# Performance work log

Measured on AMD Instinct MI355X. Metric: run time of the kernel, lower is better.

## Reference

```python
import jax, jax.numpy as jnp
import numpy as np

B, K, F, C = 256, 16, 128, 2
EPS = 1e-5


def setup_inputs() -> dict:
    key = jax.random.key(0)
    ks = jax.random.split(key, 16)
    n = lambda k, shape, s=1.0: (jax.random.normal(k, shape, dtype=jnp.float32) * s)
    return {
        "x0": n(ks[0], (B, F)),
        "x1": n(ks[1], (B, K, F)),
        "x2": n(ks[2], (B, K * K, F)),
        "x3": n(ks[3], (B, K ** 3, F)),
        "W0": n(ks[4], (2 * F, F), 0.05), "b0": n(ks[5], (F,), 0.05),
        "W1": n(ks[6], (2 * F, F), 0.05), "b1": n(ks[7], (F,), 0.05),
        "W2": n(ks[8], (2 * F, F), 0.05), "b2": n(ks[9], (F,), 0.05),
        "lin1_W": n(ks[10], (F, 8), 0.05), "lin1_b": n(ks[11], (8,), 0.05),
        "bn_gamma": jnp.ones((8,), jnp.float32), "bn_beta": jnp.zeros((8,), jnp.float32),
        "lin2_W": n(ks[12], (8, C), 0.05), "lin2_b": n(ks[13], (C,), 0.05),
    }


def _agg_mean(x):
    # block-wise mean over groups of K along dim 1: [B, N, F] -> [B, N//K, F]
    b, n_, f = x.shape
    return x.reshape(b, n_ // K, K, f).mean(axis=2)


def reference(x0, x1, x2, x3, W0, b0, W1, b1, W2, b2,
              lin1_W, lin1_b, bn_gamma, bn_beta, lin2_W, lin2_b):
    # layer i=3: mean-agg x3 blocks, concat with x2, Linear(2F->F)+ReLU
    h2 = jax.nn.relu(jnp.concatenate([_agg_mean(x3), x2], axis=2) @ W2 + b2)
    # layer i=2
    h1 = jax.nn.relu(jnp.concatenate([_agg_mean(h2), x1], axis=2) @ W1 + b1)
    # layer i=1: agg gives [B,1,F]; squeeze and concat along feature dim
    h0 = jax.nn.relu(jnp.concatenate([_agg_mean(h1)[:, 0, :], x0], axis=1) @ W0 + b0)
    # classifier head: Linear -> BatchNorm1d (training batch stats) -> Linear -> Sigmoid
    z = h0 @ lin1_W + lin1_b                       # [B, 8]
    mu = z.mean(axis=0)
    var = jnp.mean(jnp.square(z - mu), axis=0)     # biased var, as torch BN
    zn = (z - mu) * jax.lax.rsqrt(var + EPS) * bn_gamma + bn_beta
    return jax.nn.sigmoid(zn @ lin2_W + lin2_b)    # [B, C]
```

## Files before the change

kernel.cpp:

```cpp
#include <hip/hip_runtime.h>
#include <math.h>

#define NTHR 256

typedef __bf16 bf16x8 __attribute__((ext_vector_type(8)));
typedef float  f32x4  __attribute__((ext_vector_type(4)));

__device__ __forceinline__ unsigned short f2bf(float x) {
    unsigned int u = __float_as_uint(x);
    return (unsigned short)((u + 0x7fffu + ((u >> 16) & 1u)) >> 16);
}
__device__ __forceinline__ ushort4 pack4(float a, float b, float c, float d) {
    return make_ushort4(f2bf(a), f2bf(b), f2bf(c), f2bf(d));
}

template<int TM>
__global__ __launch_bounds__(NTHR, 3)
void layer_kernel(const float* __restrict__ deep,
                  const float* __restrict__ shallow,
                  const float* __restrict__ W,
                  const float* __restrict__ bias,
                  float* __restrict__ out)
{
    constexpr int MT = TM / 16;
    __shared__ unsigned short A[TM][264];
    const int t  = threadIdx.x;
    const int m0 = blockIdx.x * TM;

    {
        const int r8 = t >> 5;
        const int l  = t & 31;
        const int fo = l * 4;
        for (int rr = r8; rr < TM; rr += 8) {
            const int m = m0 + rr;
            const float4* dp = (const float4*)(deep + (size_t)m * 2048 + fo);
            float4 s = dp[0];
            #pragma unroll
            for (int k = 1; k < 16; ++k) {
                float4 v = dp[k * 32];
                s.x += v.x; s.y += v.y; s.z += v.z; s.w += v.w;
            }
            const float inv = 1.0f / 16.0f;
            float4 sh = *(const float4*)(shallow + (size_t)m * 128 + fo);
            *(ushort4*)&A[rr][fo]       = pack4(s.x * inv, s.y * inv, s.z * inv, s.w * inv);
            *(ushort4*)&A[rr][128 + fo] = pack4(sh.x, sh.y, sh.z, sh.w);
        }
    }

    const int l    = t & 63;
    const int w    = t >> 6;
    const int lo16 = l & 15;
    const int q    = l >> 4;
    const int c0   = w * 32;

    bf16x8 Bf[16];
    #pragma unroll
    for (int kt = 0; kt < 8; ++kt) {
        #pragma unroll
        for (int nt = 0; nt < 2; ++nt) {
            const float* p = W + (size_t)(kt * 32 + q * 8) * 128 + c0 + nt * 16 + lo16;
            union { unsigned short u[8]; bf16x8 v; } tmp;
            #pragma unroll
            for (int j = 0; j < 8; ++j) tmp.u[j] = f2bf(p[(size_t)j * 128]);
            Bf[kt * 2 + nt] = tmp.v;
        }
    }
    __syncthreads();

    f32x4 acc[MT][2];
    #pragma unroll
    for (int mt = 0; mt < MT; ++mt) {
        acc[mt][0] = (f32x4){0.f, 0.f, 0.f, 0.f};
        acc[mt][1] = (f32x4){0.f, 0.f, 0.f, 0.f};
    }

    #pragma unroll
    for (int kt = 0; kt < 8; ++kt) {
        #pragma unroll
        for (int mt = 0; mt < MT; ++mt) {
            bf16x8 Af = *(const bf16x8*)&A[mt * 16 + lo16][kt * 32 + q * 8];
            acc[mt][0] = __builtin_amdgcn_mfma_f32_16x16x32_bf16(Af, Bf[kt * 2 + 0], acc[mt][0], 0, 0, 0);
            acc[mt][1] = __builtin_amdgcn_mfma_f32_16x16x32_bf16(Af, Bf[kt * 2 + 1], acc[mt][1], 0, 0, 0);
        }
    }

    const float bn0 = bias[c0 + lo16];
    const float bn1 = bias[c0 + 16 + lo16];
    #pragma unroll
    for (int mt = 0; mt < MT; ++mt) {
        #pragma unroll
        for (int r = 0; r < 4; ++r) {
            const int row = m0 + mt * 16 + q * 4 + r;
            float* op = out + (size_t)row * 128;
            op[c0 + lo16]      = fmaxf(acc[mt][0][r] + bn0, 0.0f);
            op[c0 + 16 + lo16] = fmaxf(acc[mt][1][r] + bn1, 0.0f);
        }
    }
}

__global__ __launch_bounds__(NTHR)
void head_kernel(const float* __restrict__ h0,
                 const float* __restrict__ l1W,
                 const float* __restrict__ l1b,
                 const float* __restrict__ gamma,
                 const float* __restrict__ beta,
                 const float* __restrict__ l2W,
                 const float* __restrict__ l2b,
                 float* __restrict__ out)
{
    __shared__ float z[256][8];
    __shared__ float w1s[128 * 8];
    __shared__ float ps[32][8];
    __shared__ float pq[32][8];
    __shared__ float scale_s[8], shift_s[8];

    const int t  = threadIdx.x;
    const int j  = t & 7;
    const int rg = t >> 3;

    #pragma unroll
    for (int i = 0; i < 4; ++i) w1s[t * 4 + i] = l1W[t * 4 + i];
    __syncthreads();

    const float bj = l1b[j];
    for (int it = 0; it < 8; ++it) {
        const int b = it * 32 + rg;
        const float4* hr = (const float4*)(h0 + (size_t)b * 128);
        float s = bj;
        #pragma unroll
        for (int f4 = 0; f4 < 32; ++f4) {
            float4 h = hr[f4];
            s += h.x * w1s[(f4 * 4 + 0) * 8 + j];
            s += h.y * w1s[(f4 * 4 + 1) * 8 + j];
            s += h.z * w1s[(f4 * 4 + 2) * 8 + j];
            s += h.w * w1s[(f4 * 4 + 3) * 8 + j];
        }
        z[b][j] = s;
    }
    __syncthreads();

    {
        float s = 0.0f, qq = 0.0f;
        #pragma unroll
        for (int r = 0; r < 8; ++r) {
            float v = z[rg * 8 + r][j];
            s += v; qq += v * v;
        }
        ps[rg][j] = s; pq[rg][j] = qq;
    }
    __syncthreads();

    if (t < 8) {
        float s = 0.0f, qq = 0.0f;
        #pragma unroll
        for (int p = 0; p < 32; ++p) { s += ps[p][t]; qq += pq[p][t]; }
        const float mu  = s * (1.0f / 256.0f);
        const float var = qq * (1.0f / 256.0f) - mu * mu;
        const float sc  = gamma[t] * rsqrtf(var + 1e-5f);
        scale_s[t] = sc;
        shift_s[t] = beta[t] - mu * sc;
    }
    __syncthreads();

    {
        float o0 = l2b[0], o1 = l2b[1];
        #pragma unroll
        for (int jj = 0; jj < 8; ++jj) {
            const float zn = z[t][jj] * scale_s[jj] + shift_s[jj];
            o0 += zn * l2W[jj * 2 + 0];
            o1 += zn * l2W[jj * 2 + 1];
        }
        out[t * 2 + 0] = 1.0f / (1.0f + expf(-o0));
        out[t * 2 + 1] = 1.0f / (1.0f + expf(-o1));
    }
}

extern "C" void kernel_launch(void* const* d_in, const int* in_sizes, int n_in,
                              void* d_out, int out_size, void* d_ws, size_t ws_size,
                              hipStream_t stream)
{
    const float* x0    = (const float*)d_in[0];
    const float* x1    = (const float*)d_in[1];
    const float* x2    = (const float*)d_in[2];
    const float* x3    = (const float*)d_in[3];
    const float* W0    = (const float*)d_in[4];
    const float* b0    = (const float*)d_in[5];
    const float* W1    = (const float*)d_in[6];
    const float* b1    = (const float*)d_in[7];
    const float* W2    = (const float*)d_in[8];
    const float* b2    = (const float*)d_in[9];
    const float* l1W   = (const float*)d_in[10];
    const float* l1b   = (const float*)d_in[11];
    const float* gamma = (const float*)d_in[12];
    const float* beta  = (const float*)d_in[13];
    const float* l2W   = (const float*)d_in[14];
    const float* l2b   = (const float*)d_in[15];
    float* out = (float*)d_out;

    float* h2 = (float*)d_ws;
    float* h1 = h2 + (size_t)65536 * 128;
    float* h0 = h1 + (size_t)4096 * 128;

    hipLaunchKernelGGL((layer_kernel<64>), dim3(65536 / 64), dim3(NTHR), 0, stream,
                       x3, x2, W2, b2, h2);
    hipLaunchKernelGGL((layer_kernel<16>), dim3(4096 / 16), dim3(NTHR), 0, stream,
                       h2, x1, W1, b1, h1);
    hipLaunchKernelGGL((layer_kernel<16>), dim3(256 / 16), dim3(NTHR), 0, stream,
                       h1, x0, W0, b0, h0);
    hipLaunchKernelGGL(head_kernel, dim3(1), dim3(NTHR), 0, stream,
                       h0, l1W, l1b, gamma, beta, l2W, l2b, out);
}
```

Baseline: 761.8 us.

## Fuse downstream mean-aggregation into layer epilogues and use nontemporal loads

Each layer now reduces its ReLU outputs over groups of 16 rows inside the MFMA epilogue, using cross-lane shuffles, and writes only the group means. This removes the full h2/h1 intermediate writes and the 16x re-read in the next layer. The x3 stream is read with nontemporal loads, and occupancy hint rises to 4 blocks. Later layers use 64-row tiles, so launch grids are much smaller (64 and 4 blocks), which limits parallelism for those stages.

After: 732.7 us. -3.8%, faster.

```diff
diff --git a/kernel.cpp b/kernel.cpp
--- a/kernel.cpp
+++ b/kernel.cpp
@@ -5,22 +5,26 @@
 
 typedef __bf16 bf16x8 __attribute__((ext_vector_type(8)));
 typedef float  f32x4  __attribute__((ext_vector_type(4)));
+typedef float  f32x4v __attribute__((ext_vector_type(4)));
 
 __device__ __forceinline__ unsigned short f2bf(float x) {
     unsigned int u = __float_as_uint(x);
     return (unsigned short)((u + 0x7fffu + ((u >> 16) & 1u)) >> 16);
 }
-__device__ __forceinline__ ushort4 pack4(float a, float b, float c, float d) {
-    return make_ushort4(f2bf(a), f2bf(b), f2bf(c), f2bf(d));
-}
-
-template<int TM>
-__global__ __launch_bounds__(NTHR, 3)
+__device__ __forceinline__ ushort4 pack4v(f32x4v v) {
+    return make_ushort4(f2bf(v[0]), f2bf(v[1]), f2bf(v[2]), f2bf(v[3]));
+}
+__device__ __forceinline__ f32x4v ntload4(const float* p) {
+    return __builtin_nontemporal_load((const f32x4v*)p);
+}
+
+template<int TM, bool AGG_IN, bool AGG_OUT>
+__global__ __launch_bounds__(NTHR, 4)
 void layer_kernel(const float* __restrict__ deep,
-                  const float* __restrict__ shallow,
+                  const float* __restrict__ shal,
                   const float* __restrict__ W,
                   const float* __restrict__ bias,
-                  float* __restrict__ out)
+                  float* __restrict__ outp)
 {
     constexpr int MT = TM / 16;
     __shared__ unsigned short A[TM][264];
@@ -33,17 +37,20 @@
         const int fo = l * 4;
         for (int rr = r8; rr < TM; rr += 8) {
             const int m = m0 + rr;
-            const float4* dp = (const float4*)(deep + (size_t)m * 2048 + fo);
-            float4 s = dp[0];
-            #pragma unroll
-            for (int k = 1; k < 16; ++k) {
-                float4 v = dp[k * 32];
-                s.x += v.x; s.y += v.y; s.z += v.z; s.w += v.w;
+            f32x4v s, sh;
+            if (AGG_IN) {
+                const float* dp = deep + (size_t)m * 2048 + fo;
+                s = ntload4(dp);
+                #pragma unroll
+                for (int k = 1; k < 16; ++k) s += ntload4(dp + k * 128);
+                s *= (1.0f / 16.0f);
+                sh = ntload4(shal + (size_t)m * 128 + fo);
+            } else {
+                s  = *(const f32x4v*)(deep + (size_t)m * 128 + fo);
+                sh = *(const f32x4v*)(shal + (size_t)m * 128 + fo);
             }
-            const float inv = 1.0f / 16.0f;
-            float4 sh = *(const float4*)(shallow + (size_t)m * 128 + fo);
-            *(ushort4*)&A[rr][fo]       = pack4(s.x * inv, s.y * inv, s.z * inv, s.w * inv);
-            *(ushort4*)&A[rr][128 + fo] = pack4(sh.x, sh.y, sh.z, sh.w);
+            *(ushort4*)&A[rr][fo]       = pack4v(s);
+            *(ushort4*)&A[rr][128 + fo] = pack4v(sh);
         }
     }
 
@@ -73,7 +80,6 @@
         acc[mt][0] = (f32x4){0.f, 0.f, 0.f, 0.f};
         acc[mt][1] = (f32x4){0.f, 0.f, 0.f, 0.f};
     }
-
     #pragma unroll
     for (int kt = 0; kt < 8; ++kt) {
         #pragma unroll
@@ -86,14 +92,31 @@
 
     const float bn0 = bias[c0 + lo16];
     const float bn1 = bias[c0 + 16 + lo16];
-    #pragma unroll
-    for (int mt = 0; mt < MT; ++mt) {
-        #pragma unroll
-        for (int r = 0; r < 4; ++r) {
-            const int row = m0 + mt * 16 + q * 4 + r;
-            float* op = out + (size_t)row * 128;
-            op[c0 + lo16]      = fmaxf(acc[mt][0][r] + bn0, 0.0f);
-            op[c0 + 16 + lo16] = fmaxf(acc[mt][1][r] + bn1, 0.0f);
+    if (AGG_OUT) {
+        #pragma unroll
+        for (int mt = 0; mt < MT; ++mt) {
+            float v0 = 0.f, v1 = 0.f;
+            #pragma unroll
+            for (int r = 0; r < 4; ++r) {
+                v0 += fmaxf(acc[mt][0][r] + bn0, 0.0f);
+                v1 += fmaxf(acc[mt][1][r] + bn1, 0.0f);
+            }
+            v0 += __shfl_xor(v0, 16, 64); v0 += __shfl_xor(v0, 32, 64);
+            v1 += __shfl_xor(v1, 16, 64); v1 += __shfl_xor(v1, 32, 64);
+            const int g = blockIdx.x * MT + mt;
+            if (q == 0) outp[(size_t)g * 128 + c0 + lo16]      = v0 * 0.0625f;
+            if (q == 1) outp[(size_t)g * 128 + c0 + 16 + lo16] = v1 * 0.0625f;
+        }
+    } else {
+        #pragma unroll
+        for (int mt = 0; mt < MT; ++mt) {
+            #pragma unroll
+            for (int r = 0; r < 4; ++r) {
+                const int row = m0 + mt * 16 + q * 4 + r;
+                float* op = outp + (size_t)row * 128;
+                op[c0 + lo16]      = fmaxf(acc[mt][0][r] + bn0, 0.0f);
+                op[c0 + 16 + lo16] = fmaxf(acc[mt][1][r] + bn1, 0.0f);
+            }
         }
     }
 }
@@ -197,16 +220,16 @@
     const float* l2b   = (const float*)d_in[15];
     float* out = (float*)d_out;
 
-    float* h2 = (float*)d_ws;
-    float* h1 = h2 + (size_t)65536 * 128;
-    float* h0 = h1 + (size_t)4096 * 128;
-
-    hipLaunchKernelGGL((layer_kernel<64>), dim3(65536 / 64), dim3(NTHR), 0, stream,
-                       x3, x2, W2, b2, h2);
-    hipLaunchKernelGGL((layer_kernel<16>), dim3(4096 / 16), dim3(NTHR), 0, stream,
-                       h2, x1, W1, b1, h1);
-    hipLaunchKernelGGL((layer_kernel<16>), dim3(256 / 16), dim3(NTHR), 0, stream,
-                       h1, x0, W0, b0, h0);
+    float* h2m = (float*)d_ws;
+    float* h1m = h2m + (size_t)4096 * 128;
+    float* h0  = h1m + (size_t)256 * 128;
+
+    hipLaunchKernelGGL((layer_kernel<64, true, true>), dim3(65536 / 64), dim3(NTHR), 0, stream,
+                       x3, x2, W2, b2, h2m);
+    hipLaunchKernelGGL((layer_kernel<64, false, true>), dim3(4096 / 64), dim3(NTHR), 0, stream,
+                       h2m, x1, W1, b1, h1m);
+    hipLaunchKernelGGL((layer_kernel<64, false, false>), dim3(256 / 64), dim3(NTHR), 0, stream,
+                       h1m, x0, W0, b0, h0);
     hipLaunchKernelGGL(head_kernel, dim3(1), dim3(NTHR), 0, stream,
                        h0, l1W, l1b, gamma, beta, l2W, l2b, out);
 }
```
